# Kernel optimization log

Hardware: AMD Instinct MI355X
Metric: run time of the kernel (lower is better)

Reference implementation:

```python
import math
import jax, jax.numpy as jnp
import numpy as np

B, T, C, HS = 4, 4096, 1024, 64  # batch, seq, n_embd, head_size=n_embd//n_head

def setup_inputs() -> dict:
    key = jax.random.key(0)
    k0, k1, k2, k3 = jax.random.split(key, 4)
    x = jax.random.normal(k0, (B, T, C), dtype=jnp.float32)
    Wq = jax.random.normal(k1, (C, HS), dtype=jnp.float32) * 0.02
    Wk = jax.random.normal(k2, (C, HS), dtype=jnp.float32) * 0.02
    Wv = jax.random.normal(k3, (C, HS), dtype=jnp.float32) * 0.02
    return {"x": x, "Wq": Wq, "Wk": Wk, "Wv": Wv}

def reference(x, Wq, Wk, Wv):
    b, t, c = x.shape
    q = x @ Wq                                   # [B,T,hs]
    k = x @ Wk                                   # [B,T,hs]
    v = x @ Wv                                   # [B,T,hs]
    wei = jnp.einsum('btd,bsd->bts', q, k)       # [B,T,T] raw scores
    row_sums = wei.sum(axis=-1)                  # [B,T]
    k_sel = math.ceil(t / 2)                     # static: t known at trace time
    _, idx = jax.lax.top_k(row_sums, k_sel)      # [B,k_sel]
    idx = jnp.sort(idx, axis=1)
    # gather selected score rows: [B,k_sel,T]
    half_wei = jnp.take_along_axis(wei, idx[:, :, None], axis=1)
    # causal mask rows gathered from tril: tril[idx[b,i], j] == (j <= idx[b,i])
    half_mask = jnp.arange(t)[None, None, :] <= idx[:, :, None]  # [B,k_sel,T] bool
    half_wei = half_wei * (c ** -0.5)            # NOTE: scaled by n_embd, as in source
    half_wei = jnp.where(half_mask, half_wei, -jnp.inf)
    att = jax.nn.softmax(half_wei, axis=-1)      # [B,k_sel,T]
    out = att @ v                                # [B,k_sel,hs]
    return out
```

## Files before the change

kernel.cpp:

```cpp
#include <hip/hip_runtime.h>
#include <math.h>

#define BB 4
#define TT 4096
#define CC 1024
#define HS 64
#define KSEL 2048
#define NEG (-1e30f)
#define NSPL 16
#define SWLOG 8
#define SW 256

typedef float f32x4 __attribute__((ext_vector_type(4)));
typedef short short8 __attribute__((ext_vector_type(8)));

__device__ __forceinline__ unsigned short f2bf(float f) {
  union { float f; unsigned int u; } c;
  c.f = f;
  const unsigned int u = c.u;
  return (unsigned short)((u + 0x7FFFu + ((u >> 16) & 1u)) >> 16);
}

__device__ __forceinline__ unsigned cvtpk(float lo, float hi) {
  unsigned r;
  asm("v_cvt_pk_bf16_f32 %0, %1, %2" : "=v"(r) : "v"(lo), "v"(hi));
  return r;
}

__global__ __launch_bounds__(256) void conv_w(const float* __restrict__ Wq,
                                              const float* __restrict__ Wk,
                                              const float* __restrict__ Wv,
                                              unsigned short* __restrict__ wbf) {
  const int gid = blockIdx.x * 256 + threadIdx.x;
  const int kt = gid / 768;
  const int rem = gid - kt * 768;
  const int nt = rem >> 6, lane = rem & 63;
  const int col = nt * 16 + (lane & 15);
  const float* W = (col < 64) ? Wq : ((col < 128) ? Wk : Wv);
  const int cl = col & 63;
  const int k0 = kt * 32 + (lane >> 4) * 8;
  unsigned short tmp[8];
#pragma unroll
  for (int i = 0; i < 8; i++) tmp[i] = f2bf(W[(size_t)(k0 + i) * HS + cl]);
  uint4 o;
  o.x = tmp[0] | ((unsigned)tmp[1] << 16);
  o.y = tmp[2] | ((unsigned)tmp[3] << 16);
  o.z = tmp[4] | ((unsigned)tmp[5] << 16);
  o.w = tmp[6] | ((unsigned)tmp[7] << 16);
  *(uint4*)(wbf + (size_t)gid * 8) = o;
}

#define PR 32
__global__ __launch_bounds__(256) void fusedproj(
    const float* __restrict__ x, const unsigned short* __restrict__ wbf,
    float* __restrict__ xsum, unsigned short* __restrict__ qbf,
    unsigned short* __restrict__ kbf, unsigned short* __restrict__ vtbf) {
  __shared__ unsigned short Xs[PR][256];
  __shared__ float xsred[4][256];
  const int rb = blockIdx.x;
  const size_t r0 = (size_t)rb * PR;
  const int tid = threadIdx.x;
  const int wid = tid >> 6, lane = tid & 63;
  const int lhi = lane >> 4, llo = lane & 15;
  const int mt = wid >> 1, nh = wid & 1;
  const int cl = tid & 63, rg = tid >> 6;
  const int bidx = rb >> 7;

  f32x4 acc[6];
#pragma unroll
  for (int n = 0; n < 6; n++) acc[n] = (f32x4){0.f, 0.f, 0.f, 0.f};

  float4 pf[8];
#pragma unroll
  for (int rr = 0; rr < 8; rr++)
    pf[rr] = *(const float4*)(x + (r0 + rg * 8 + rr) * CC + cl * 4);

  for (int ch = 0; ch < 4; ch++) {
    float ps0 = 0.f, ps1 = 0.f, ps2 = 0.f, ps3 = 0.f;
#pragma unroll
    for (int rr = 0; rr < 8; rr++) {
      const int row = rg * 8 + rr;
      float4 v = pf[rr];
      ps0 += v.x; ps1 += v.y; ps2 += v.z; ps3 += v.w;
      *(uint2*)((char*)&Xs[0][0] + row * 512 +
                ((((cl >> 1) ^ (row & 7))) << 4) + ((cl & 1) << 3)) =
          make_uint2(cvtpk(v.x, v.y), cvtpk(v.z, v.w));
    }
    xsred[rg][cl * 4 + 0] = ps0;
    xsred[rg][cl * 4 + 1] = ps1;
    xsred[rg][cl * 4 + 2] = ps2;
    xsred[rg][cl * 4 + 3] = ps3;
    __syncthreads();
    if (ch < 3) {
#pragma unroll
      for (int rr = 0; rr < 8; rr++)
        pf[rr] = *(const float4*)(x + (r0 + rg * 8 + rr) * CC +
                                  (ch + 1) * 256 + cl * 4);
    }
    atomicAdd(&xsum[bidx * CC + ch * 256 + tid],
              xsred[0][tid] + xsred[1][tid] + xsred[2][tid] + xsred[3][tid]);
    const int row = mt * 16 + llo;
#pragma unroll
    for (int ktl = 0; ktl < 8; ktl++) {
      short8 af = *(const short8*)((const char*)&Xs[0][0] + row * 512 +
                                   ((((ktl << 2) + lhi) ^ (row & 7)) << 4));
      const unsigned short* bp =
          wbf + (((size_t)(ch * 8 + ktl) * 12 + nh * 6) * 64 + lane) * 8;
#pragma unroll
      for (int n = 0; n < 6; n++) {
        short8 bf = *(const short8*)(bp + n * 64 * 8);
        acc[n] = __builtin_amdgcn_mfma_f32_16x16x32_bf16(af, bf, acc[n], 0, 0, 0);
      }
    }
    __syncthreads();
  }
  const int rbg = (int)r0 + mt * 16 + lhi * 4;
#pragma unroll
  for (int n = 0; n < 6; n++) {
    const int col = (nh * 6 + n) * 16 + llo;
    const int mat = col >> 6, cl2 = col & 63;
    if (mat == 0) {
#pragma unroll
      for (int r = 0; r < 4; r++)
        qbf[(size_t)(rbg + r) * HS + cl2] = f2bf(acc[n][r] * 0.03125f);
    } else if (mat == 1) {
#pragma unroll
      for (int r = 0; r < 4; r++)
        kbf[(size_t)(rbg + r) * HS + cl2] = f2bf(acc[n][r]);
    } else {
      const int bb = rbg >> 12, tloc = rbg & (TT - 1);
      *(uint2*)(vtbf + ((size_t)bb * HS + cl2) * TT + tloc) =
          make_uint2(cvtpk(acc[n][0], acc[n][1]), cvtpk(acc[n][2], acc[n][3]));
    }
  }
}

__global__ __launch_bounds__(512) void rowsums_x(
    const float* __restrict__ x, const float* __restrict__ Wq,
    const float* __restrict__ Wk, const float* __restrict__ xsum,
    float* __restrict__ rs) {
  __shared__ float xsl[CC];
  __shared__ float kred[8][HS];
  __shared__ float ksl[HS];
  __shared__ float wl[CC];
  const int g = blockIdx.x;
  const int tid = threadIdx.x;
  const int b = g >> 6;
  *(float2*)(xsl + tid * 2) = *(const float2*)(xsum + b * CC + tid * 2);
  __syncthreads();
  {
    const int g8 = tid >> 6, d = tid & 63;
    const float* wkp = Wk + (size_t)(g8 * 128) * HS + d;
    float s = 0.f;
    for (int c = 0; c < 128; c++) s += xsl[g8 * 128 + c] * wkp[(size_t)c * HS];
    kred[g8][d] = s;
  }
  __syncthreads();
  if (tid < 64) {
    float s = 0.f;
#pragma unroll
    for (int g8 = 0; g8 < 8; g8++) s += kred[g8][tid];
    ksl[tid] = s;
  }
  __syncthreads();
#pragma unroll
  for (int p = 0; p < 2; p++) {
    const int c = tid * 2 + p;
    const float* wqp = Wq + (size_t)c * HS;
    float s = 0.f;
#pragma unroll
    for (int d4 = 0; d4 < 16; d4++) {
      float4 a = *(const float4*)(wqp + d4 * 4);
      float4 kk = *(const float4*)(ksl + d4 * 4);
      s += a.x * kk.x + a.y * kk.y + a.z * kk.z + a.w * kk.w;
    }
    wl[c] = s;
  }
  __syncthreads();
  const size_t row = (size_t)g * 64 + (tid >> 3);
  const int qu = tid & 7;
  const float* xr = x + row * CC + qu * 128;
  const float* wr = wl + qu * 128;
  float s = 0.f;
  for (int e = 0; e < 32; e++) {
    float4 v = *(const float4*)(xr + e * 4);
    float4 w4 = *(const float4*)(wr + e * 4);
    s += v.x * w4.x + v.y * w4.y + v.z * w4.z + v.w * w4.w;
  }
  s += __shfl_xor(s, 1);
  s += __shfl_xor(s, 2);
  s += __shfl_xor(s, 4);
  if (qu == 0) rs[row] = s;
}

__global__ __launch_bounds__(256) void rankk(const float* __restrict__ rs,
                                             int* __restrict__ flag) {
  __shared__ float rl[TT];
  const int g = blockIdx.x;
  const int b = g >> 7, chunk = g & 127;
  const int tid = threadIdx.x;
  const float* rsb = rs + (size_t)b * TT;
  for (int e = tid; e < TT / 4; e += 256)
    *(float4*)(rl + e * 4) = *(const float4*)(rsb + e * 4);
  __syncthreads();
  const int cand = tid >> 3, qu = tid & 7;
  const int t = chunk * 32 + cand;
  const float my = rl[t];
  int cnt = 0;
  for (int e = 0; e < 128; e++) {
    const int s = qu * 512 + e * 4;
    float4 v = *(const float4*)(rl + s);
    cnt += (v.x > my) || (v.x == my && (s + 0) < t);
    cnt += (v.y > my) || (v.y == my && (s + 1) < t);
    cnt += (v.z > my) || (v.z == my && (s + 2) < t);
    cnt += (v.w > my) || (v.w == my && (s + 3) < t);
  }
  cnt += __shfl_xor(cnt, 1);
  cnt += __shfl_xor(cnt, 2);
  cnt += __shfl_xor(cnt, 4);
  if (qu == 0) flag[(size_t)b * TT + t] = (cnt < KSEL) ? 1 : 0;
}

__global__ __launch_bounds__(256) void compact(const int* __restrict__ flag,
                                               int* __restrict__ idx) {
  __shared__ int sums[256];
  const int b = blockIdx.x;
  const int tid = threadIdx.x;
  const int* fb = flag + (size_t)b * TT;
  const int base = tid * 16;
  int f[16];
  int cnt = 0;
#pragma unroll
  for (int e = 0; e < 16; e++) { f[e] = fb[base + e]; cnt += f[e]; }
  sums[tid] = cnt;
  __syncthreads();
  for (int d = 1; d < 256; d <<= 1) {
    int v = (tid >= d) ? sums[tid - d] : 0;
    __syncthreads();
    sums[tid] += v;
    __syncthreads();
  }
  int pos = sums[tid] - cnt;
#pragma unroll
  for (int e = 0; e < 16; e++)
    if (f[e]) idx[(size_t)b * KSEL + (pos++)] = base + e;
}

struct KF { short8 a0, a1, b0, b1; };
struct VF { short8 v0, v1, v2, v3; };

__global__ __launch_bounds__(256) void attn_mfma(
    const unsigned short* __restrict__ qbf,
    const unsigned short* __restrict__ kbf,
    const unsigned short* __restrict__ vtbf, const int* __restrict__ idx,
    float* __restrict__ pl, float* __restrict__ pacc) {
  __shared__ unsigned short P_lds[4][32][40];
  const int rb = blockIdx.x;
  const int zz = blockIdx.y;
  const int b = blockIdx.z;
  const int tid = threadIdx.x;
  const int wid = tid >> 6, lane = tid & 63;
  const int s = zz * 4 + wid;
  const size_t rbase = (size_t)b * KSEL + rb * 32;
  const int tmaxblk = idx[rbase + 31];
  const int jlo = s << SWLOG;
  if (jlo > tmaxblk) return;

  const int lhi = lane >> 4, llo = lane & 15;
  const int trow0 = idx[rbase + llo];
  const int trow1 = idx[rbase + 16 + llo];
  short8 qf[2][2];
  {
    const unsigned short* qp0 = qbf + ((size_t)b * TT + trow0) * HS + lhi * 8;
    const unsigned short* qp1 = qbf + ((size_t)b * TT + trow1) * HS + lhi * 8;
    qf[0][0] = *(const short8*)(qp0);
    qf[0][1] = *(const short8*)(qp0 + 32);
    qf[1][0] = *(const short8*)(qp1);
    qf[1][1] = *(const short8*)(qp1 + 32);
  }
  f32x4 o[2][4];
#pragma unroll
  for (int mtt = 0; mtt < 2; mtt++)
#pragma unroll
    for (int n = 0; n < 4; n++) o[mtt][n] = (f32x4){0.f, 0.f, 0.f, 0.f};
  float lsum[2] = {0.f, 0.f};

  const unsigned short* kb = kbf + (size_t)b * TT * HS;
  const unsigned short* vb = vtbf + (size_t)b * HS * TT;
  const int jend = min(tmaxblk + 1, jlo + SW);

  auto loadK = [&](int j0) {
    KF K;
    const unsigned short* kp = kb + (size_t)(j0 + llo) * HS + lhi * 8;
    K.a0 = *(const short8*)(kp);
    K.a1 = *(const short8*)(kp + 32);
    K.b0 = *(const short8*)(kp + 16 * HS);
    K.b1 = *(const short8*)(kp + 16 * HS + 32);
    return K;
  };
  auto loadV = [&](int j0) {
    VF V;
    const unsigned short* vp = vb + (size_t)llo * TT + j0 + lhi * 8;
    V.v0 = *(const short8*)(vp);
    V.v1 = *(const short8*)(vp + 16 * TT);
    V.v2 = *(const short8*)(vp + 32 * TT);
    V.v3 = *(const short8*)(vp + 48 * TT);
    return V;
  };

  auto body = [&](int j0, const KF& K, const VF& V) {
    f32x4 sc[2][2];
#pragma unroll
    for (int mtt = 0; mtt < 2; mtt++) {
      f32x4 a = (f32x4){0.f, 0.f, 0.f, 0.f};
      a = __builtin_amdgcn_mfma_f32_16x16x32_bf16(K.a0, qf[mtt][0], a, 0, 0, 0);
      a = __builtin_amdgcn_mfma_f32_16x16x32_bf16(K.a1, qf[mtt][1], a, 0, 0, 0);
      sc[mtt][0] = a;
      f32x4 c = (f32x4){0.f, 0.f, 0.f, 0.f};
      c = __builtin_amdgcn_mfma_f32_16x16x32_bf16(K.b0, qf[mtt][0], c, 0, 0, 0);
      c = __builtin_amdgcn_mfma_f32_16x16x32_bf16(K.b1, qf[mtt][1], c, 0, 0, 0);
      sc[mtt][1] = c;
    }
#pragma unroll
    for (int mtt = 0; mtt < 2; mtt++) {
      const int tr = (mtt == 0) ? trow0 : trow1;
      float p[8];
#pragma unroll
      for (int kt = 0; kt < 2; kt++)
#pragma unroll
        for (int r = 0; r < 4; r++) {
          const int kk = j0 + kt * 16 + lhi * 4 + r;
          const float e = __expf(sc[mtt][kt][r]);
          p[kt * 4 + r] = (kk <= tr) ? e : 0.f;
        }
      lsum[mtt] += ((p[0] + p[1]) + (p[2] + p[3])) +
                   ((p[4] + p[5]) + (p[6] + p[7]));
      *(uint2*)&P_lds[wid][mtt * 16 + llo][lhi * 4] =
          make_uint2(cvtpk(p[0], p[1]), cvtpk(p[2], p[3]));
      *(uint2*)&P_lds[wid][mtt * 16 + llo][16 + lhi * 4] =
          make_uint2(cvtpk(p[4], p[5]), cvtpk(p[6], p[7]));
    }
    short8 pa0 = *(const short8*)&P_lds[wid][llo][lhi * 8];
    short8 pa1 = *(const short8*)&P_lds[wid][16 + llo][lhi * 8];
    o[0][0] = __builtin_amdgcn_mfma_f32_16x16x32_bf16(pa0, V.v0, o[0][0], 0, 0, 0);
    o[1][0] = __builtin_amdgcn_mfma_f32_16x16x32_bf16(pa1, V.v0, o[1][0], 0, 0, 0);
    o[0][1] = __builtin_amdgcn_mfma_f32_16x16x32_bf16(pa0, V.v1, o[0][1], 0, 0, 0);
    o[1][1] = __builtin_amdgcn_mfma_f32_16x16x32_bf16(pa1, V.v1, o[1][1], 0, 0, 0);
    o[0][2] = __builtin_amdgcn_mfma_f32_16x16x32_bf16(pa0, V.v2, o[0][2], 0, 0, 0);
    o[1][2] = __builtin_amdgcn_mfma_f32_16x16x32_bf16(pa1, V.v2, o[1][2], 0, 0, 0);
    o[0][3] = __builtin_amdgcn_mfma_f32_16x16x32_bf16(pa0, V.v3, o[0][3], 0, 0, 0);
    o[1][3] = __builtin_amdgcn_mfma_f32_16x16x32_bf16(pa1, V.v3, o[1][3], 0, 0, 0);
  };

  int j0 = jlo;
  KF ka = loadK(j0), kb2;
  VF va = loadV(j0), vb2;
  for (;;) {
    if (j0 + 32 < jend) { kb2 = loadK(j0 + 32); vb2 = loadV(j0 + 32); }
    body(j0, ka, va);
    j0 += 32;
    if (j0 >= jend) break;
    if (j0 + 32 < jend) { ka = loadK(j0 + 32); va = loadV(j0 + 32); }
    body(j0, kb2, vb2);
    j0 += 32;
    if (j0 >= jend) break;
  }

  lsum[0] += __shfl_xor(lsum[0], 16);
  lsum[0] += __shfl_xor(lsum[0], 32);
  lsum[1] += __shfl_xor(lsum[1], 16);
  lsum[1] += __shfl_xor(lsum[1], 32);
  if (lane < 16) {
    pl[(rbase + llo) * NSPL + s] = lsum[0];
    pl[(rbase + 16 + llo) * NSPL + s] = lsum[1];
  }
#pragma unroll
  for (int mtt = 0; mtt < 2; mtt++)
#pragma unroll
    for (int r = 0; r < 4; r++) {
      const size_t rowi = rbase + mtt * 16 + lhi * 4 + r;
#pragma unroll
      for (int n = 0; n < 4; n++)
        pacc[(rowi * NSPL + s) * HS + n * 16 + llo] = o[mtt][n][r];
    }
}

__global__ __launch_bounds__(256) void attn_combine(
    const float* __restrict__ pl, const float* __restrict__ pacc,
    const int* __restrict__ idx, float* __restrict__ out) {
  const int b = blockIdx.x;
  const int i0 = blockIdx.y * 32;
  const int tid = threadIdx.x;
  const int r = tid >> 3, dg = tid & 7;
  const size_t rowi = (size_t)b * KSEL + i0 + r;
  const int t_r = idx[rowi];
  const int ns = (t_r >> SWLOG) + 1;
  float L = 0.f;
  float o[8] = {0.f, 0.f, 0.f, 0.f, 0.f, 0.f, 0.f, 0.f};
  for (int s = 0; s < ns; s++) {
    L += pl[rowi * NSPL + s];
    const float* pa = pacc + (rowi * NSPL + s) * HS + dg * 8;
    float4 a0 = *(const float4*)(pa);
    float4 a1 = *(const float4*)(pa + 4);
    o[0] += a0.x; o[1] += a0.y; o[2] += a0.z; o[3] += a0.w;
    o[4] += a1.x; o[5] += a1.y; o[6] += a1.z; o[7] += a1.w;
  }
  const float invl = 1.0f / L;
  float* op = out + rowi * HS + dg * 8;
  *(float4*)(op) = make_float4(o[0] * invl, o[1] * invl, o[2] * invl, o[3] * invl);
  *(float4*)(op + 4) = make_float4(o[4] * invl, o[5] * invl, o[6] * invl, o[7] * invl);
}

extern "C" void kernel_launch(void* const* d_in, const int* in_sizes, int n_in,
                              void* d_out, int out_size, void* d_ws,
                              size_t ws_size, hipStream_t stream) {
  const float* x = (const float*)d_in[0];
  const float* Wq = (const float*)d_in[1];
  const float* Wk = (const float*)d_in[2];
  const float* Wv = (const float*)d_in[3];
  float* out = (float*)d_out;

  float* wsf = (float*)d_ws;
  float* pacc = wsf;
  float* xsum = wsf;
  float* rs = xsum + 4096;
  int* flag = (int*)(rs + 16384);
  unsigned short* wbf = (unsigned short*)(flag + 16384);
  unsigned short* qbf = (unsigned short*)(pacc + 8388608);
  unsigned short* kbf = qbf + 1048576;
  unsigned short* vtbf = kbf + 1048576;
  int* idxp = (int*)(vtbf + 1048576);
  float* pl = (float*)(idxp + 8192);

  hipMemsetAsync(xsum, 0, BB * CC * sizeof(float), stream);
  conv_w<<<96, 256, 0, stream>>>(Wq, Wk, Wv, wbf);
  fusedproj<<<512, 256, 0, stream>>>(x, wbf, xsum, qbf, kbf, vtbf);
  rowsums_x<<<256, 512, 0, stream>>>(x, Wq, Wk, xsum, rs);
  rankk<<<512, 256, 0, stream>>>(rs, flag);
  compact<<<BB, 256, 0, stream>>>(flag, idxp);
  attn_mfma<<<dim3(64, 4, BB), 256, 0, stream>>>(qbf, kbf, vtbf, idxp, pl, pacc);
  attn_combine<<<dim3(BB, 64), 256, 0, stream>>>(pl, pacc, idxp, out);
}
```

Baseline: 128.6 us.

## Replace split-K partial buffers with atomic accumulation into output and fold memset

Attention splits now atomically add their unnormalized outputs and row sums directly into the output and a per-row L buffer, so the large pacc workspace and the combine pass go away. A light normalize kernel divides by L afterwards. Zeroing of xsum, L and out moves into the weight-conversion kernel, which removes the memset launch. The projection kernel also drops to 16 rows per block with twice as many blocks. The cost is float atomic contention on out and nondeterministic summation order.

```diff
diff --git a/kernel.cpp b/kernel.cpp
--- a/kernel.cpp
+++ b/kernel.cpp
@@ -6,7 +6,6 @@
 #define CC 1024
 #define HS 64
 #define KSEL 2048
-#define NEG (-1e30f)
 #define NSPL 16
 #define SWLOG 8
 #define SW 256
@@ -30,8 +29,18 @@
 __global__ __launch_bounds__(256) void conv_w(const float* __restrict__ Wq,
                                               const float* __restrict__ Wk,
                                               const float* __restrict__ Wv,
-                                              unsigned short* __restrict__ wbf) {
+                                              unsigned short* __restrict__ wbf,
+                                              float* __restrict__ xsum,
+                                              float* __restrict__ L,
+                                              float* __restrict__ out) {
   const int gid = blockIdx.x * 256 + threadIdx.x;
+  const float4 z4 = make_float4(0.f, 0.f, 0.f, 0.f);
+#pragma unroll
+  for (int e = 0; e < 4; e++) ((float4*)out)[gid + e * 32768] = z4;
+  if (gid < 2048) ((float4*)L)[gid] = z4;
+  if (gid < 1024) ((float4*)xsum)[gid] = z4;
+
+  if (gid >= 24576) return;
   const int kt = gid / 768;
   const int rem = gid - kt * 768;
   const int nt = rem >> 6, lane = rem & 63;
@@ -50,7 +59,7 @@
   *(uint4*)(wbf + (size_t)gid * 8) = o;
 }
 
-#define PR 32
+#define PR 16
 __global__ __launch_bounds__(256) void fusedproj(
     const float* __restrict__ x, const unsigned short* __restrict__ wbf,
     float* __restrict__ xsum, unsigned short* __restrict__ qbf,
@@ -62,24 +71,23 @@
   const int tid = threadIdx.x;
   const int wid = tid >> 6, lane = tid & 63;
   const int lhi = lane >> 4, llo = lane & 15;
-  const int mt = wid >> 1, nh = wid & 1;
   const int cl = tid & 63, rg = tid >> 6;
-  const int bidx = rb >> 7;
-
-  f32x4 acc[6];
-#pragma unroll
-  for (int n = 0; n < 6; n++) acc[n] = (f32x4){0.f, 0.f, 0.f, 0.f};
-
-  float4 pf[8];
-#pragma unroll
-  for (int rr = 0; rr < 8; rr++)
-    pf[rr] = *(const float4*)(x + (r0 + rg * 8 + rr) * CC + cl * 4);
+  const int bidx = rb >> 8;
+
+  f32x4 acc[3];
+#pragma unroll
+  for (int n = 0; n < 3; n++) acc[n] = (f32x4){0.f, 0.f, 0.f, 0.f};
+
+  float4 pf[4];
+#pragma unroll
+  for (int rr = 0; rr < 4; rr++)
+    pf[rr] = *(const float4*)(x + (r0 + rg * 4 + rr) * CC + cl * 4);
 
   for (int ch = 0; ch < 4; ch++) {
     float ps0 = 0.f, ps1 = 0.f, ps2 = 0.f, ps3 = 0.f;
 #pragma unroll
-    for (int rr = 0; rr < 8; rr++) {
-      const int row = rg * 8 + rr;
+    for (int rr = 0; rr < 4; rr++) {
+      const int row = rg * 4 + rr;
       float4 v = pf[rr];
       ps0 += v.x; ps1 += v.y; ps2 += v.z; ps3 += v.w;
       *(uint2*)((char*)&Xs[0][0] + row * 512 +
@@ -93,31 +101,30 @@
     __syncthreads();
     if (ch < 3) {
 #pragma unroll
-      for (int rr = 0; rr < 8; rr++)
-        pf[rr] = *(const float4*)(x + (r0 + rg * 8 + rr) * CC +
+      for (int rr = 0; rr < 4; rr++)
+        pf[rr] = *(const float4*)(x + (r0 + rg * 4 + rr) * CC +
                                   (ch + 1) * 256 + cl * 4);
     }
     atomicAdd(&xsum[bidx * CC + ch * 256 + tid],
               xsred[0][tid] + xsred[1][tid] + xsred[2][tid] + xsred[3][tid]);
-    const int row = mt * 16 + llo;
 #pragma unroll
     for (int ktl = 0; ktl < 8; ktl++) {
-      short8 af = *(const short8*)((const char*)&Xs[0][0] + row * 512 +
-                                   ((((ktl << 2) + lhi) ^ (row & 7)) << 4));
+      short8 af = *(const short8*)((const char*)&Xs[0][0] + llo * 512 +
+                                   ((((ktl << 2) + lhi) ^ (llo & 7)) << 4));
       const unsigned short* bp =
-          wbf + (((size_t)(ch * 8 + ktl) * 12 + nh * 6) * 64 + lane) * 8;
-#pragma unroll
-      for (int n = 0; n < 6; n++) {
+          wbf + (((size_t)(ch * 8 + ktl) * 12 + wid * 3) * 64 + lane) * 8;
+#pragma unroll
+      for (int n = 0; n < 3; n++) {
         short8 bf = *(const short8*)(bp + n * 64 * 8);
         acc[n] = __builtin_amdgcn_mfma_f32_16x16x32_bf16(af, bf, acc[n], 0, 0, 0);
       }
     }
     __syncthreads();
   }
-  const int rbg = (int)r0 + mt * 16 + lhi * 4;
-#pragma unroll
-  for (int n = 0; n < 6; n++) {
-    const int col = (nh * 6 + n) * 16 + llo;
+  const int rbg = (int)r0 + lhi * 4;
+#pragma unroll
+  for (int n = 0; n < 3; n++) {
+    const int col = (wid * 3 + n) * 16 + llo;
     const int mat = col >> 6, cl2 = col & 63;
     if (mat == 0) {
 #pragma unroll
@@ -253,7 +260,7 @@
     const unsigned short* __restrict__ qbf,
     const unsigned short* __restrict__ kbf,
     const unsigned short* __restrict__ vtbf, const int* __restrict__ idx,
-    float* __restrict__ pl, float* __restrict__ pacc) {
+    float* __restrict__ L, float* __restrict__ out) {
   __shared__ unsigned short P_lds[4][32][40];
   const int rb = blockIdx.x;
   const int zz = blockIdx.y;
@@ -371,44 +378,26 @@
   lsum[1] += __shfl_xor(lsum[1], 16);
   lsum[1] += __shfl_xor(lsum[1], 32);
   if (lane < 16) {
-    pl[(rbase + llo) * NSPL + s] = lsum[0];
-    pl[(rbase + 16 + llo) * NSPL + s] = lsum[1];
+    atomicAdd(&L[rbase + llo], lsum[0]);
+    atomicAdd(&L[rbase + 16 + llo], lsum[1]);
   }
 #pragma unroll
   for (int mtt = 0; mtt < 2; mtt++)
 #pragma unroll
     for (int r = 0; r < 4; r++) {
-      const size_t rowi = rbase + mtt * 16 + lhi * 4 + r;
-#pragma unroll
-      for (int n = 0; n < 4; n++)
-        pacc[(rowi * NSPL + s) * HS + n * 16 + llo] = o[mtt][n][r];
-    }
-}
-
-__global__ __launch_bounds__(256) void attn_combine(
-    const float* __restrict__ pl, const float* __restrict__ pacc,
-    const int* __restrict__ idx, float* __restrict__ out) {
-  const int b = blockIdx.x;
-  const int i0 = blockIdx.y * 32;
-  const int tid = threadIdx.x;
-  const int r = tid >> 3, dg = tid & 7;
-  const size_t rowi = (size_t)b * KSEL + i0 + r;
-  const int t_r = idx[rowi];
-  const int ns = (t_r >> SWLOG) + 1;
-  float L = 0.f;
-  float o[8] = {0.f, 0.f, 0.f, 0.f, 0.f, 0.f, 0.f, 0.f};
-  for (int s = 0; s < ns; s++) {
-    L += pl[rowi * NSPL + s];
-    const float* pa = pacc + (rowi * NSPL + s) * HS + dg * 8;
-    float4 a0 = *(const float4*)(pa);
-    float4 a1 = *(const float4*)(pa + 4);
-    o[0] += a0.x; o[1] += a0.y; o[2] += a0.z; o[3] += a0.w;
-    o[4] += a1.x; o[5] += a1.y; o[6] += a1.z; o[7] += a1.w;
-  }
-  const float invl = 1.0f / L;
-  float* op = out + rowi * HS + dg * 8;
-  *(float4*)(op) = make_float4(o[0] * invl, o[1] * invl, o[2] * invl, o[3] * invl);
-  *(float4*)(op + 4) = make_float4(o[4] * invl, o[5] * invl, o[6] * invl, o[7] * invl);
+      float* op = out + (rbase + mtt * 16 + lhi * 4 + r) * HS;
+#pragma unroll
+      for (int n = 0; n < 4; n++) atomicAdd(op + n * 16 + llo, o[mtt][n][r]);
+    }
+}
+
+__global__ __launch_bounds__(256) void normalize(const float* __restrict__ L,
+                                                 float* __restrict__ out) {
+  const int gid = blockIdx.x * 256 + threadIdx.x;
+  const float invl = 1.0f / L[gid >> 4];
+  float4 v = ((float4*)out)[gid];
+  v.x *= invl; v.y *= invl; v.z *= invl; v.w *= invl;
+  ((float4*)out)[gid] = v;
 }
 
 extern "C" void kernel_launch(void* const* d_in, const int* in_sizes, int n_in,
@@ -421,23 +410,21 @@
   float* out = (float*)d_out;
 
   float* wsf = (float*)d_ws;
-  float* pacc = wsf;
   float* xsum = wsf;
   float* rs = xsum + 4096;
   int* flag = (int*)(rs + 16384);
-  unsigned short* wbf = (unsigned short*)(flag + 16384);
-  unsigned short* qbf = (unsigned short*)(pacc + 8388608);
+  float* L = (float*)(flag + 16384);
+  unsigned short* wbf = (unsigned short*)(L + 8192);
+  unsigned short* qbf = wbf + 196608;
   unsigned short* kbf = qbf + 1048576;
   unsigned short* vtbf = kbf + 1048576;
   int* idxp = (int*)(vtbf + 1048576);
-  float* pl = (float*)(idxp + 8192);
-
-  hipMemsetAsync(xsum, 0, BB * CC * sizeof(float), stream);
-  conv_w<<<96, 256, 0, stream>>>(Wq, Wk, Wv, wbf);
-  fusedproj<<<512, 256, 0, stream>>>(x, wbf, xsum, qbf, kbf, vtbf);
+
+  conv_w<<<128, 256, 0, stream>>>(Wq, Wk, Wv, wbf, xsum, L, out);
+  fusedproj<<<1024, 256, 0, stream>>>(x, wbf, xsum, qbf, kbf, vtbf);
   rowsums_x<<<256, 512, 0, stream>>>(x, Wq, Wk, xsum, rs);
   rankk<<<512, 256, 0, stream>>>(rs, flag);
   compact<<<BB, 256, 0, stream>>>(flag, idxp);
-  attn_mfma<<<dim3(64, 4, BB), 256, 0, stream>>>(qbf, kbf, vtbf, idxp, pl, pacc);
-  attn_combine<<<dim3(BB, 64), 256, 0, stream>>>(pl, pacc, idxp, out);
-}
+  attn_mfma<<<dim3(64, 4, BB), 256, 0, stream>>>(qbf, kbf, vtbf, idxp, L, out);
+  normalize<<<512, 256, 0, stream>>>(L, out);
+}
```

Measured after the change: 134.3 us. 1.04x slower.
